# Performance work log

Hardware: AMD Instinct MI355X
Metric: run time of the kernel (lower is better)

The kernel has to match this reference:

```python
import jax, jax.numpy as jnp
import numpy as np

B, N, NC, T, C, H = 8, 16, 16, 64, 512, 8


def setup_inputs() -> dict:
    key = jax.random.key(0)
    ks = jax.random.split(key, 7)
    s = 1.0 / np.sqrt(C)  # ~kaiming-uniform scale for Linear weights
    x = jax.random.normal(ks[0], (B, N, T, C), dtype=jnp.float32)
    c = jax.random.normal(ks[1], (B, NC, T, C), dtype=jnp.float32)
    mask = jax.random.randint(ks[2], (B, N * T, (N + NC) * T), 0, 2).astype(bool)
    Wq = jax.random.normal(ks[3], (C, C), dtype=jnp.float32) * s  # [out, in], torch Linear layout
    Wk = jax.random.normal(ks[4], (C, C), dtype=jnp.float32) * s
    Wv = jax.random.normal(ks[5], (C, C), dtype=jnp.float32) * s
    Wp = jax.random.normal(ks[6], (C, C), dtype=jnp.float32) * s
    return {"x": x, "c": c, "mask": mask, "Wq": Wq, "Wk": Wk, "Wv": Wv, "Wp": Wp}


def reference(x, c, mask, Wq, Wk, Wv, Wp):
    Bx, Nx, Tx, Cx = x.shape
    Dh = Cx // H
    kv_in = jnp.concatenate([x, c], axis=1)           # hybrid: [B, N+NC, T, C]
    Nk = kv_in.shape[1]
    # torch Linear: y = x @ W.T  -> einsum '...c,dc->...d'
    q = jnp.einsum('bntc,dc->bntd', x, Wq).reshape(Bx, Nx * Tx, H, Dh).transpose(0, 2, 1, 3)
    k = jnp.einsum('bntc,dc->bntd', kv_in, Wk).reshape(Bx, Nk * Tx, H, Dh).transpose(0, 2, 1, 3)
    v = jnp.einsum('bntc,dc->bntd', kv_in, Wv).reshape(Bx, Nk * Tx, H, Dh).transpose(0, 2, 1, 3)
    att = jnp.einsum('bhqd,bhkd->bhqk', q, k) * (1.0 / np.sqrt(Dh))  # [B,H,NT,NkT]
    att = jnp.where(mask[:, None, :, :], -jnp.inf, att)
    att = jax.nn.softmax(att, axis=-1)
    y = jnp.einsum('bhqk,bhkd->bhqd', att, v)          # [B,H,NT,Dh]
    y = y.transpose(0, 2, 1, 3).reshape(Bx, Nx * Tx, Cx)
    y = jnp.einsum('btc,dc->btd', y, Wp)
    return y.reshape(Bx, Nx, Tx, Cx)
```

## Files before the change

kernel.cpp:

```cpp
#include <hip/hip_runtime.h>
#include <hip/hip_bf16.h>
#include <stdint.h>

typedef __bf16 v8bf __attribute__((ext_vector_type(8)));
typedef short v4s __attribute__((ext_vector_type(4)));
typedef float f32x4 __attribute__((ext_vector_type(4)));

__device__ __forceinline__ void gload_lds16(const void* g, void* l) {
    __builtin_amdgcn_global_load_lds(
        (const __attribute__((address_space(1))) void*)g,
        (__attribute__((address_space(3))) void*)l, 16, 0, 0);
}

__device__ __forceinline__ unsigned short f2bf(float f) {
    __hip_bfloat16 h = __float2bfloat16(f);
    return __builtin_bit_cast(unsigned short, h);
}

__device__ __forceinline__ float andf(float e, int m) {
    return __builtin_bit_cast(float, __builtin_bit_cast(unsigned int, e) & (unsigned int)m);
}

#define SBIT(w, off, ioff) (((int)((w) << (ioff))) >> 31)

#define WAITV4_BAR() asm volatile("s_waitcnt vmcnt(4)\n\ts_barrier" ::: "memory")
#define WAITV0_BAR() asm volatile("s_waitcnt vmcnt(0)\n\ts_barrier" ::: "memory")
#define RAW_BAR() asm volatile("s_barrier" ::: "memory")

__device__ __forceinline__ f32x4 mfma16x16x16bf(v4s a, v4s b, f32x4 c) {
#if __has_builtin(__builtin_amdgcn_mfma_f32_16x16x16bf16_1k)
    return __builtin_amdgcn_mfma_f32_16x16x16bf16_1k(a, b, c, 0, 0, 0);
#elif __has_builtin(__builtin_amdgcn_mfma_f32_16x16x16_bf16)
    return __builtin_amdgcn_mfma_f32_16x16x16_bf16(a, b, c, 0, 0, 0);
#else
    asm("s_nop 1\n\t"
        "v_mfma_f32_16x16x16_bf16 %0, %1, %2, %0\n\t"
        "s_nop 7\n\ts_nop 3"
        : "+v"(c) : "v"(a), "v"(b));
    return c;
#endif
}

__global__ __launch_bounds__(256) void cvt_xcw(const float* __restrict__ x,
                                               const float* __restrict__ c,
                                               const float* __restrict__ wq,
                                               const float* __restrict__ wk,
                                               const float* __restrict__ wv,
                                               const float* __restrict__ wp,
                                               __hip_bfloat16* __restrict__ xc,
                                               __hip_bfloat16* __restrict__ wout) {
    int bid = blockIdx.x;
    if (bid < 8192) {
        int i = bid * 256 + threadIdx.x;
        long e = (long)i * 4;
        int b = (int)(e >> 20);
        int rem = (int)(e & ((1 << 20) - 1));
        int r = rem >> 9;
        int col = rem & 511;
        const float* src = (r < 1024) ? (x + ((long)b << 19) + (long)r * 512 + col)
                                      : (c + ((long)b << 19) + (long)(r - 1024) * 512 + col);
        float4 v = *(const float4*)src;
        ushort4 o;
        o.x = f2bf(v.x); o.y = f2bf(v.y); o.z = f2bf(v.z); o.w = f2bf(v.w);
        ((ushort4*)xc)[i] = o;
    } else {
        int i = (bid - 8192) * 256 + threadIdx.x;
        int e = i * 4;
        int w = e >> 18;
        int off = e & ((1 << 18) - 1);
        const float* src = (w == 0 ? wq : w == 1 ? wk : w == 2 ? wv : wp) + off;
        float4 val = *(const float4*)src;
        ushort4 o;
        o.x = f2bf(val.x); o.y = f2bf(val.y); o.z = f2bf(val.z); o.w = f2bf(val.w);
        ((ushort4*)wout)[i] = o;
    }
}

__global__ __launch_bounds__(256) void cvt_mask(const int* __restrict__ mask,
                                                unsigned long long* __restrict__ mbt) {
    int t = threadIdx.x;
    long base = (long)blockIdx.x * 1024;
#pragma unroll
    for (int j = 0; j < 4; j++) {
        long i = base + j * 256 + t;
        int v = mask[i] != 0;
        unsigned long long bits = __ballot(v);
        if ((t & 63) == 0) {
            int b = (int)(i >> 21);
            int q = (int)((i >> 11) & 1023);
            int word = (int)((i >> 6) & 31);
            mbt[((long)b * 32 + word) * 1024 + q] = bits;
        }
    }
}

__global__ __launch_bounds__(256) void gemm_qkv(const __hip_bfloat16* __restrict__ A,
                                                const __hip_bfloat16* __restrict__ Bw,
                                                __hip_bfloat16* __restrict__ Qw,
                                                __hip_bfloat16* __restrict__ Kw,
                                                __hip_bfloat16* __restrict__ Vtw) {
    __shared__ union {
        struct { __hip_bfloat16 As[2][128 * 32]; __hip_bfloat16 Bs[2][128 * 32]; } s;
        __hip_bfloat16 T[64 * 136];
    } u;
    const int tid = threadIdx.x;
    const int wave = tid >> 6, lane = tid & 63;
    const int m0 = blockIdx.x * 128, n0 = blockIdx.y * 128;

    const int la = lane >> 2;
    const int kc = (lane & 3) * 8;
    const long ga0 = (long)(m0 + wave * 16 + la) * 512 + kc;
    const long ga1 = (long)(m0 + (wave + 4) * 16 + la) * 512 + kc;
    const long gb0 = (long)(n0 + wave * 16 + la) * 512 + kc;
    const long gb1 = (long)(n0 + (wave + 4) * 16 + la) * 512 + kc;

    f32x4 acc[4][4] = {};
    const int mw = (wave & 1) * 64, nw = (wave >> 1) * 64;
    const int lrow = lane & 15, lk = (lane >> 4) * 8;

    gload_lds16(A + ga0, &u.s.As[0][wave * 512]);
    gload_lds16(A + ga1, &u.s.As[0][(wave + 4) * 512]);
    gload_lds16(Bw + gb0, &u.s.Bs[0][wave * 512]);
    gload_lds16(Bw + gb1, &u.s.Bs[0][(wave + 4) * 512]);

    for (int it = 0; it < 16; ++it) {
        const int cur = it & 1;
        if (it < 15) {
            const int k0 = (it + 1) * 32;
            gload_lds16(A + ga0 + k0, &u.s.As[cur ^ 1][wave * 512]);
            gload_lds16(A + ga1 + k0, &u.s.As[cur ^ 1][(wave + 4) * 512]);
            gload_lds16(Bw + gb0 + k0, &u.s.Bs[cur ^ 1][wave * 512]);
            gload_lds16(Bw + gb1 + k0, &u.s.Bs[cur ^ 1][(wave + 4) * 512]);
            WAITV4_BAR();
        } else {
            WAITV0_BAR();
        }
        v8bf a[4], b[4];
#pragma unroll
        for (int i = 0; i < 4; i++) {
            a[i] = *(const v8bf*)&u.s.As[cur][(mw + i * 16 + lrow) * 32 + lk];
            b[i] = *(const v8bf*)&u.s.Bs[cur][(nw + i * 16 + lrow) * 32 + lk];
        }
        __builtin_amdgcn_s_setprio(1);
#pragma unroll
        for (int mi = 0; mi < 4; mi++)
#pragma unroll
            for (int ni = 0; ni < 4; ni++)
                acc[mi][ni] = __builtin_amdgcn_mfma_f32_16x16x32_bf16(a[mi], b[ni], acc[mi][ni], 0, 0, 0);
        __builtin_amdgcn_s_setprio(0);
        RAW_BAR();
    }

    const int lq = lane >> 4;
    if (blockIdx.y < 8) {
#pragma unroll
        for (int mi = 0; mi < 4; mi++)
#pragma unroll
            for (int ni = 0; ni < 4; ni++)
#pragma unroll
                for (int r = 0; r < 4; r++) {
                    int grow = m0 + mw + mi * 16 + lq * 4 + r;
                    int gcol = n0 + nw + ni * 16 + lrow;
                    int w = gcol >> 9, g9 = gcol & 511;
                    int h = g9 >> 6, dh = g9 & 63;
                    int b_ = grow >> 11, rr = grow & 2047;
                    float val = acc[mi][ni][r];
                    if (w == 0) {
                        if (rr < 1024)
                            Qw[((long)(b_ * 8 + h) * 1024 + rr) * 64 + dh] =
                                __float2bfloat16(val * 0.1803368801f);
                    } else {
                        Kw[((long)(b_ * 8 + h) * 2048 + rr) * 64 + dh] = __float2bfloat16(val);
                    }
                }
    } else {
        const int no = (blockIdx.y - 8) * 128;
        const int b_ = m0 >> 11, rrb = m0 & 2047;
#pragma unroll
        for (int pass = 0; pass < 2; ++pass) {
            __syncthreads();
            if ((wave >> 1) == pass) {
#pragma unroll
                for (int mi = 0; mi < 4; mi++)
#pragma unroll
                    for (int ni = 0; ni < 4; ni++) {
                        int n_l = ni * 16 + lrow;
                        int m_l = mw + mi * 16 + lq * 4;
                        ushort4 pk;
                        pk.x = f2bf(acc[mi][ni][0]); pk.y = f2bf(acc[mi][ni][1]);
                        pk.z = f2bf(acc[mi][ni][2]); pk.w = f2bf(acc[mi][ni][3]);
                        *(ushort4*)&u.T[n_l * 136 + m_l] = pk;
                    }
            }
            __syncthreads();
#pragma unroll
            for (int i = 0; i < 4; i++) {
                int sI = tid + i * 256;
                int n_l = sI >> 4, ch = sI & 15;
                int ng = no + pass * 64 + n_l;
                int h = ng >> 6, dh = ng & 63;
                uint4 v = *(const uint4*)&u.T[n_l * 136 + ch * 8];
                *(uint4*)&Vtw[((long)(b_ * 8 + h) * 64 + dh) * 2048 + rrb + ch * 8] = v;
            }
        }
    }
}

__global__ __launch_bounds__(256) void gemm_out(const __hip_bfloat16* __restrict__ A,
                                                const __hip_bfloat16* __restrict__ Bw,
                                                float* __restrict__ outp) {
    __shared__ __hip_bfloat16 As[2][128 * 32];
    __shared__ __hip_bfloat16 Bs[2][128 * 32];
    const int tid = threadIdx.x;
    const int wave = tid >> 6, lane = tid & 63;
    const int m0 = blockIdx.x * 128, n0 = blockIdx.y * 128;

    const int la = lane >> 2;
    const int kc = (lane & 3) * 8;
    const long ga0 = (long)(m0 + wave * 16 + la) * 512 + kc;
    const long ga1 = (long)(m0 + (wave + 4) * 16 + la) * 512 + kc;
    const long gb0 = (long)(n0 + wave * 16 + la) * 512 + kc;
    const long gb1 = (long)(n0 + (wave + 4) * 16 + la) * 512 + kc;

    f32x4 acc[4][4] = {};
    const int mw = (wave & 1) * 64, nw = (wave >> 1) * 64;
    const int lrow = lane & 15, lk = (lane >> 4) * 8;

    gload_lds16(A + ga0, &As[0][wave * 512]);
    gload_lds16(A + ga1, &As[0][(wave + 4) * 512]);
    gload_lds16(Bw + gb0, &Bs[0][wave * 512]);
    gload_lds16(Bw + gb1, &Bs[0][(wave + 4) * 512]);

    for (int it = 0; it < 16; ++it) {
        const int cur = it & 1;
        if (it < 15) {
            const int k0 = (it + 1) * 32;
            gload_lds16(A + ga0 + k0, &As[cur ^ 1][wave * 512]);
            gload_lds16(A + ga1 + k0, &As[cur ^ 1][(wave + 4) * 512]);
            gload_lds16(Bw + gb0 + k0, &Bs[cur ^ 1][wave * 512]);
            gload_lds16(Bw + gb1 + k0, &Bs[cur ^ 1][(wave + 4) * 512]);
            WAITV4_BAR();
        } else {
            WAITV0_BAR();
        }
        v8bf a[4], b[4];
#pragma unroll
        for (int i = 0; i < 4; i++) {
            a[i] = *(const v8bf*)&As[cur][(mw + i * 16 + lrow) * 32 + lk];
            b[i] = *(const v8bf*)&Bs[cur][(nw + i * 16 + lrow) * 32 + lk];
        }
        __builtin_amdgcn_s_setprio(1);
#pragma unroll
        for (int mi = 0; mi < 4; mi++)
#pragma unroll
            for (int ni = 0; ni < 4; ni++)
                acc[mi][ni] = __builtin_amdgcn_mfma_f32_16x16x32_bf16(a[mi], b[ni], acc[mi][ni], 0, 0, 0);
        __builtin_amdgcn_s_setprio(0);
        RAW_BAR();
    }

    const int lq = lane >> 4;
#pragma unroll
    for (int mi = 0; mi < 4; mi++)
#pragma unroll
        for (int ni = 0; ni < 4; ni++)
#pragma unroll
            for (int r = 0; r < 4; r++) {
                int grow = m0 + mw + mi * 16 + lq * 4 + r;
                int gcol = n0 + nw + ni * 16 + lrow;
                outp[(long)grow * 512 + gcol] = acc[mi][ni][r];
            }
}

__global__ __launch_bounds__(256) void flash(const __hip_bfloat16* __restrict__ Q,
                                             const __hip_bfloat16* __restrict__ K,
                                             const __hip_bfloat16* __restrict__ Vt,
                                             const unsigned long long* __restrict__ Mbt,
                                             __hip_bfloat16* __restrict__ Y) {
    constexpr int LDT = 72;
    __shared__ __hip_bfloat16 Ks[2][64 * LDT];
    __shared__ __hip_bfloat16 Vts[2][64 * LDT];

    const int L = blockIdx.x;
    const int b = L & 7, qt = (L >> 3) & 15, h = L >> 7;
    const int bh = b * 8 + h;
    const int tid = threadIdx.x, w = tid >> 6, lane = tid & 63;
    const int lcol = lane & 15, lq = lane >> 4;

    const __hip_bfloat16* Qp = Q + ((long)bh * 1024 + qt * 64 + w * 16 + lcol) * 64 + lq * 8;
    const __hip_bfloat16* Kg = K + (long)bh * 2048 * 64;
    const __hip_bfloat16* Vg = Vt + (long)bh * 64 * 2048;
    const unsigned long long* Mp = Mbt + (long)b * 32 * 1024 + qt * 64 + w * 16 + lcol;

    const int u0 = tid, u1 = tid + 256;
    const int r0 = u0 >> 3, p0 = u0 & 7;
    const int r1 = u1 >> 3, p1 = u1 & 7;

    int ioff[8];
#pragma unroll
    for (int jj = 0; jj < 8; jj++)
        ioff[jj] = 31 - ((jj >> 2) * 16 + lq * 4 + (jj & 3));

    v8bf bq0 = *(const v8bf*)(Qp);
    v8bf bq1 = *(const v8bf*)(Qp + 32);

    f32x4 O[4] = {};
    f32x4 Osum = {};
    const v4s bones = {(short)0x3F80, (short)0x3F80, (short)0x3F80, (short)0x3F80};

    unsigned long long mword = Mp[0];
    {
        const uint4* ksrc = (const uint4*)Kg;
        uint4 k0 = ksrc[u0], k1 = ksrc[u1];
        uint4 v0 = *(const uint4*)(Vg + (long)r0 * 2048 + p0 * 8);
        uint4 v1 = *(const uint4*)(Vg + (long)r1 * 2048 + p1 * 8);
        *(uint4*)&Ks[0][r0 * LDT + p0 * 8] = k0;
        *(uint4*)&Ks[0][r1 * LDT + p1 * 8] = k1;
        *(uint4*)&Vts[0][r0 * LDT + p0 * 8] = v0;
        *(uint4*)&Vts[0][r1 * LDT + p1 * 8] = v1;
    }
    __syncthreads();

    int cur = 0;
    for (int kt = 0; kt < 32; kt++) {
        const unsigned int kw_lo = ~(unsigned int)mword;
        const unsigned int kw_hi = ~(unsigned int)(mword >> 32);

        uint4 nk0, nk1, nv0, nv1;
        if (kt < 31) {
            const uint4* ksrc = (const uint4*)(Kg + ((kt + 1) << 12));
            nk0 = ksrc[u0];
            nk1 = ksrc[u1];
            nv0 = *(const uint4*)(Vg + (long)r0 * 2048 + (kt + 1) * 64 + p0 * 8);
            nv1 = *(const uint4*)(Vg + (long)r1 * 2048 + (kt + 1) * 64 + p1 * 8);
            mword = Mp[(long)(kt + 1) * 1024];
        }

        const __hip_bfloat16* Kb = Ks[cur];
        const __hip_bfloat16* Vb = Vts[cur];
#pragma unroll
        for (int nt = 0; nt < 4; nt++) {
            v8bf ak0 = *(const v8bf*)&Kb[(nt * 16 + lcol) * LDT + lq * 8];
            v8bf ak1 = *(const v8bf*)&Kb[(nt * 16 + lcol) * LDT + 32 + lq * 8];
            f32x4 st = {};
            __builtin_amdgcn_s_setprio(1);
            st = __builtin_amdgcn_mfma_f32_16x16x32_bf16(ak0, bq0, st, 0, 0, 0);
            st = __builtin_amdgcn_mfma_f32_16x16x32_bf16(ak1, bq1, st, 0, 0, 0);
            __builtin_amdgcn_s_setprio(0);
            const unsigned int kw = (nt < 2) ? kw_lo : kw_hi;
            const int base = (nt & 1) * 4;
            float e0 = andf(__builtin_amdgcn_exp2f(st[0]), SBIT(kw, , ioff[base + 0]));
            float e1 = andf(__builtin_amdgcn_exp2f(st[1]), SBIT(kw, , ioff[base + 1]));
            float e2 = andf(__builtin_amdgcn_exp2f(st[2]), SBIT(kw, , ioff[base + 2]));
            float e3 = andf(__builtin_amdgcn_exp2f(st[3]), SBIT(kw, , ioff[base + 3]));
            __hip_bfloat162 lo = __float22bfloat162_rn(make_float2(e0, e1));
            __hip_bfloat162 hi = __float22bfloat162_rn(make_float2(e2, e3));
            uint2 pku;
            __builtin_memcpy(&pku.x, &lo, 4);
            __builtin_memcpy(&pku.y, &hi, 4);
            v4s pa = __builtin_bit_cast(v4s, pku);
            __builtin_amdgcn_s_setprio(1);
            Osum = mfma16x16x16bf(pa, bones, Osum);
#pragma unroll
            for (int nd = 0; nd < 4; nd++) {
                v4s bv = *(const v4s*)&Vb[(nd * 16 + lcol) * LDT + nt * 16 + lq * 4];
                O[nd] = mfma16x16x16bf(pa, bv, O[nd]);
            }
            __builtin_amdgcn_s_setprio(0);
        }

        if (kt < 31) {
            __hip_bfloat16* Kw_ = Ks[cur ^ 1];
            __hip_bfloat16* Vw_ = Vts[cur ^ 1];
            *(uint4*)&Kw_[r0 * LDT + p0 * 8] = nk0;
            *(uint4*)&Kw_[r1 * LDT + p1 * 8] = nk1;
            *(uint4*)&Vw_[r0 * LDT + p0 * 8] = nv0;
            *(uint4*)&Vw_[r1 * LDT + p1 * 8] = nv1;
        }
        __syncthreads();
        cur ^= 1;
    }

    float inv[4];
#pragma unroll
    for (int r = 0; r < 4; r++) inv[r] = 1.f / Osum[r];

    __hip_bfloat16* Yp = Y + ((long)b * 1024 + qt * 64 + w * 16) * 512 + h * 64 + lcol;
#pragma unroll
    for (int nd = 0; nd < 4; nd++)
#pragma unroll
        for (int r = 0; r < 4; r++)
            Yp[(long)(lq * 4 + r) * 512 + nd * 16] = __float2bfloat16(O[nd][r] * inv[r]);
}

extern "C" void kernel_launch(void* const* d_in, const int* in_sizes, int n_in,
                              void* d_out, int out_size, void* d_ws, size_t ws_size,
                              hipStream_t stream) {
    const float* x = (const float*)d_in[0];
    const float* c = (const float*)d_in[1];
    const int* mask = (const int*)d_in[2];
    const float* Wq = (const float*)d_in[3];
    const float* Wk = (const float*)d_in[4];
    const float* Wv = (const float*)d_in[5];
    const float* Wp = (const float*)d_in[6];

    char* ws = (char*)d_ws;
    __hip_bfloat16* xc  = (__hip_bfloat16*)(ws);
    __hip_bfloat16* Wbf = (__hip_bfloat16*)(ws + 16777216);
    __hip_bfloat16* Qw  = (__hip_bfloat16*)(ws + 18874368);
    __hip_bfloat16* Kw  = (__hip_bfloat16*)(ws + 27262976);
    __hip_bfloat16* Vtw = (__hip_bfloat16*)(ws + 44040192);
    __hip_bfloat16* Yb  = (__hip_bfloat16*)(ws + 60817408);
    unsigned long long* Mbp = (unsigned long long*)(ws);

    cvt_xcw<<<9216, 256, 0, stream>>>(x, c, Wq, Wk, Wv, Wp, xc, Wbf);
    gemm_qkv<<<dim3(128, 12), 256, 0, stream>>>(xc, Wbf, Qw, Kw, Vtw);
    cvt_mask<<<16384, 256, 0, stream>>>(mask, Mbp);
    flash<<<1024, 256, 0, stream>>>(Qw, Kw, Vtw, Mbp, Yb);
    gemm_out<<<dim3(64, 4), 256, 0, stream>>>(Yb, Wbf + 3 * 262144, (float*)d_out);
}
```

Measured before the change: 262.1 us.

## Load K tiles directly into swizzled LDS and compute softmax row sums with shuffles

The projection kernel now writes K with an XOR chunk swizzle per row, so the flash kernel can copy K tiles straight from global to LDS with global_load_lds. This removes the register staging and LDS stores for K and avoids bank conflicts without padding. The softmax denominator is now accumulated in scalar registers and reduced with cross-lane shuffles, replacing an extra MFMA per tile. Vt loading stays register-staged, and the direct LDS loads rely on the existing barrier for completion.

```diff
diff --git a/kernel.cpp b/kernel.cpp
--- a/kernel.cpp
+++ b/kernel.cpp
@@ -21,7 +21,7 @@
     return __builtin_bit_cast(float, __builtin_bit_cast(unsigned int, e) & (unsigned int)m);
 }
 
-#define SBIT(w, off, ioff) (((int)((w) << (ioff))) >> 31)
+#define SBIT(w, ioff) (((int)((w) << (ioff))) >> 31)
 
 #define WAITV4_BAR() asm volatile("s_waitcnt vmcnt(4)\n\ts_barrier" ::: "memory")
 #define WAITV0_BAR() asm volatile("s_waitcnt vmcnt(0)\n\ts_barrier" ::: "memory")
@@ -170,7 +170,8 @@
                             Qw[((long)(b_ * 8 + h) * 1024 + rr) * 64 + dh] =
                                 __float2bfloat16(val * 0.1803368801f);
                     } else {
-                        Kw[((long)(b_ * 8 + h) * 2048 + rr) * 64 + dh] = __float2bfloat16(val);
+                        Kw[((long)(b_ * 8 + h) * 2048 + rr) * 64 + (dh ^ ((rr & 7) << 3))] =
+                            __float2bfloat16(val);
                     }
                 }
     } else {
@@ -278,7 +279,7 @@
                                              const unsigned long long* __restrict__ Mbt,
                                              __hip_bfloat16* __restrict__ Y) {
     constexpr int LDT = 72;
-    __shared__ __hip_bfloat16 Ks[2][64 * LDT];
+    __shared__ __hip_bfloat16 KsL[2][64 * 64];
     __shared__ __hip_bfloat16 Vts[2][64 * LDT];
 
     const int L = blockIdx.x;
@@ -292,30 +293,35 @@
     const __hip_bfloat16* Vg = Vt + (long)bh * 64 * 2048;
     const unsigned long long* Mp = Mbt + (long)b * 32 * 1024 + qt * 64 + w * 16 + lcol;
 
-    const int u0 = tid, u1 = tid + 256;
-    const int r0 = u0 >> 3, p0 = u0 & 7;
+    const int u1 = tid + 256;
+    const int r0 = tid >> 3, p0 = tid & 7;
     const int r1 = u1 >> 3, p1 = u1 & 7;
+    const __hip_bfloat16* Vp0 = Vg + (long)r0 * 2048 + p0 * 8;
+    const __hip_bfloat16* Vp1 = Vg + (long)r1 * 2048 + p1 * 8;
+
+    const __hip_bfloat16* Kc0 = Kg + (w * 64 + lane) * 8;
+    const __hip_bfloat16* Kc1 = Kc0 + 2048;
 
     int ioff[8];
 #pragma unroll
     for (int jj = 0; jj < 8; jj++)
         ioff[jj] = 31 - ((jj >> 2) * 16 + lq * 4 + (jj & 3));
 
+    const int ksw0 = (lq ^ (lcol & 7)) * 8;
+    const int ksw1 = ((lq + 4) ^ (lcol & 7)) * 8;
+
     v8bf bq0 = *(const v8bf*)(Qp);
     v8bf bq1 = *(const v8bf*)(Qp + 32);
 
     f32x4 O[4] = {};
-    f32x4 Osum = {};
-    const v4s bones = {(short)0x3F80, (short)0x3F80, (short)0x3F80, (short)0x3F80};
+    float lsum = 0.f;
 
     unsigned long long mword = Mp[0];
     {
-        const uint4* ksrc = (const uint4*)Kg;
-        uint4 k0 = ksrc[u0], k1 = ksrc[u1];
-        uint4 v0 = *(const uint4*)(Vg + (long)r0 * 2048 + p0 * 8);
-        uint4 v1 = *(const uint4*)(Vg + (long)r1 * 2048 + p1 * 8);
-        *(uint4*)&Ks[0][r0 * LDT + p0 * 8] = k0;
-        *(uint4*)&Ks[0][r1 * LDT + p1 * 8] = k1;
+        gload_lds16(Kc0, &KsL[0][w * 512]);
+        gload_lds16(Kc1, &KsL[0][2048 + w * 512]);
+        uint4 v0 = *(const uint4*)(Vp0);
+        uint4 v1 = *(const uint4*)(Vp1);
         *(uint4*)&Vts[0][r0 * LDT + p0 * 8] = v0;
         *(uint4*)&Vts[0][r1 * LDT + p1 * 8] = v1;
     }
@@ -326,22 +332,22 @@
         const unsigned int kw_lo = ~(unsigned int)mword;
         const unsigned int kw_hi = ~(unsigned int)(mword >> 32);
 
-        uint4 nk0, nk1, nv0, nv1;
+        uint4 nv0, nv1;
         if (kt < 31) {
-            const uint4* ksrc = (const uint4*)(Kg + ((kt + 1) << 12));
-            nk0 = ksrc[u0];
-            nk1 = ksrc[u1];
-            nv0 = *(const uint4*)(Vg + (long)r0 * 2048 + (kt + 1) * 64 + p0 * 8);
-            nv1 = *(const uint4*)(Vg + (long)r1 * 2048 + (kt + 1) * 64 + p1 * 8);
+            gload_lds16(Kc0 + (kt + 1) * 4096, &KsL[cur ^ 1][w * 512]);
+            gload_lds16(Kc1 + (kt + 1) * 4096, &KsL[cur ^ 1][2048 + w * 512]);
+            nv0 = *(const uint4*)(Vp0 + (kt + 1) * 64);
+            nv1 = *(const uint4*)(Vp1 + (kt + 1) * 64);
             mword = Mp[(long)(kt + 1) * 1024];
         }
 
-        const __hip_bfloat16* Kb = Ks[cur];
+        const __hip_bfloat16* Kb = KsL[cur];
         const __hip_bfloat16* Vb = Vts[cur];
 #pragma unroll
         for (int nt = 0; nt < 4; nt++) {
-            v8bf ak0 = *(const v8bf*)&Kb[(nt * 16 + lcol) * LDT + lq * 8];
-            v8bf ak1 = *(const v8bf*)&Kb[(nt * 16 + lcol) * LDT + 32 + lq * 8];
+            const int rowb = (nt * 16 + lcol) * 64;
+            v8bf ak0 = *(const v8bf*)&Kb[rowb + ksw0];
+            v8bf ak1 = *(const v8bf*)&Kb[rowb + ksw1];
             f32x4 st = {};
             __builtin_amdgcn_s_setprio(1);
             st = __builtin_amdgcn_mfma_f32_16x16x32_bf16(ak0, bq0, st, 0, 0, 0);
@@ -349,10 +355,11 @@
             __builtin_amdgcn_s_setprio(0);
             const unsigned int kw = (nt < 2) ? kw_lo : kw_hi;
             const int base = (nt & 1) * 4;
-            float e0 = andf(__builtin_amdgcn_exp2f(st[0]), SBIT(kw, , ioff[base + 0]));
-            float e1 = andf(__builtin_amdgcn_exp2f(st[1]), SBIT(kw, , ioff[base + 1]));
-            float e2 = andf(__builtin_amdgcn_exp2f(st[2]), SBIT(kw, , ioff[base + 2]));
-            float e3 = andf(__builtin_amdgcn_exp2f(st[3]), SBIT(kw, , ioff[base + 3]));
+            float e0 = andf(__builtin_amdgcn_exp2f(st[0]), SBIT(kw, ioff[base + 0]));
+            float e1 = andf(__builtin_amdgcn_exp2f(st[1]), SBIT(kw, ioff[base + 1]));
+            float e2 = andf(__builtin_amdgcn_exp2f(st[2]), SBIT(kw, ioff[base + 2]));
+            float e3 = andf(__builtin_amdgcn_exp2f(st[3]), SBIT(kw, ioff[base + 3]));
+            lsum += (e0 + e1) + (e2 + e3);
             __hip_bfloat162 lo = __float22bfloat162_rn(make_float2(e0, e1));
             __hip_bfloat162 hi = __float22bfloat162_rn(make_float2(e2, e3));
             uint2 pku;
@@ -360,7 +367,6 @@
             __builtin_memcpy(&pku.y, &hi, 4);
             v4s pa = __builtin_bit_cast(v4s, pku);
             __builtin_amdgcn_s_setprio(1);
-            Osum = mfma16x16x16bf(pa, bones, Osum);
 #pragma unroll
             for (int nd = 0; nd < 4; nd++) {
                 v4s bv = *(const v4s*)&Vb[(nd * 16 + lcol) * LDT + nt * 16 + lq * 4];
@@ -370,10 +376,7 @@
         }
 
         if (kt < 31) {
-            __hip_bfloat16* Kw_ = Ks[cur ^ 1];
             __hip_bfloat16* Vw_ = Vts[cur ^ 1];
-            *(uint4*)&Kw_[r0 * LDT + p0 * 8] = nk0;
-            *(uint4*)&Kw_[r1 * LDT + p1 * 8] = nk1;
             *(uint4*)&Vw_[r0 * LDT + p0 * 8] = nv0;
             *(uint4*)&Vw_[r1 * LDT + p1 * 8] = nv1;
         }
@@ -381,9 +384,12 @@
         cur ^= 1;
     }
 
+    float s = lsum;
+    s += __shfl_xor(s, 16);
+    s += __shfl_xor(s, 32);
     float inv[4];
 #pragma unroll
-    for (int r = 0; r < 4; r++) inv[r] = 1.f / Osum[r];
+    for (int r = 0; r < 4; r++) inv[r] = 1.f / __shfl(s, lq * 4 + r);
 
     __hip_bfloat16* Yp = Y + ((long)b * 1024 + qt * 64 + w * 16) * 512 + h * 64 + lcol;
 #pragma unroll
```

Result: slower. 271.5 us (+3.6%).

## Stage Q/K epilogue through LDS, skip dead Q tiles, sum softmax denominators in VALU

Applied to the files above, without the earlier changes.

The Q/K epilogue of the QKV GEMM is staged through a padded LDS tile so global stores are 16-byte vectors instead of scattered 2-byte writes. Q-column blocks whose rows fall in the context half now exit early instead of computing and discarding. In attention, the row-sum MFMA against a ones vector is replaced by an fp32 VALU accumulation plus cross-lane shuffles. The mask bits are inverted at conversion time so a single v_bfe_i32 produces the keep-mask directly. The costs are an extra LDS round trip and barriers in the epilogue, and per-element adds and shuffles in the attention loop.

```diff
diff --git a/kernel.cpp b/kernel.cpp
--- a/kernel.cpp
+++ b/kernel.cpp
@@ -5,6 +5,7 @@
 typedef __bf16 v8bf __attribute__((ext_vector_type(8)));
 typedef short v4s __attribute__((ext_vector_type(4)));
 typedef float f32x4 __attribute__((ext_vector_type(4)));
+typedef float f32x2 __attribute__((ext_vector_type(2)));
 
 __device__ __forceinline__ void gload_lds16(const void* g, void* l) {
     __builtin_amdgcn_global_load_lds(
@@ -21,7 +22,11 @@
     return __builtin_bit_cast(float, __builtin_bit_cast(unsigned int, e) & (unsigned int)m);
 }
 
-#define SBIT(w, off, ioff) (((int)((w) << (ioff))) >> 31)
+__device__ __forceinline__ int sbit(unsigned int w, int off) {
+    int m;
+    asm("v_bfe_i32 %0, %1, %2, 1" : "=v"(m) : "v"(w), "v"(off));
+    return m;
+}
 
 #define WAITV4_BAR() asm volatile("s_waitcnt vmcnt(4)\n\ts_barrier" ::: "memory")
 #define WAITV0_BAR() asm volatile("s_waitcnt vmcnt(0)\n\ts_barrier" ::: "memory")
@@ -83,7 +88,7 @@
 #pragma unroll
     for (int j = 0; j < 4; j++) {
         long i = base + j * 256 + t;
-        int v = mask[i] != 0;
+        int v = mask[i] == 0;
         unsigned long long bits = __ballot(v);
         if ((t & 63) == 0) {
             int b = (int)(i >> 21);
@@ -101,11 +106,15 @@
                                                 __hip_bfloat16* __restrict__ Vtw) {
     __shared__ union {
         struct { __hip_bfloat16 As[2][128 * 32]; __hip_bfloat16 Bs[2][128 * 32]; } s;
-        __hip_bfloat16 T[64 * 136];
+        __hip_bfloat16 T[64 * 138];
     } u;
     const int tid = threadIdx.x;
     const int wave = tid >> 6, lane = tid & 63;
     const int m0 = blockIdx.x * 128, n0 = blockIdx.y * 128;
+
+    const bool isQ = (blockIdx.y < 4);
+    const int rr_base = m0 & 2047;
+    if (isQ && rr_base >= 1024) return;
 
     const int la = lane >> 2;
     const int kc = (lane & 3) * 8;
@@ -152,30 +161,43 @@
     }
 
     const int lq = lane >> 4;
+    const int b_ = m0 >> 11;
     if (blockIdx.y < 8) {
-#pragma unroll
-        for (int mi = 0; mi < 4; mi++)
-#pragma unroll
-            for (int ni = 0; ni < 4; ni++)
-#pragma unroll
-                for (int r = 0; r < 4; r++) {
-                    int grow = m0 + mw + mi * 16 + lq * 4 + r;
-                    int gcol = n0 + nw + ni * 16 + lrow;
-                    int w = gcol >> 9, g9 = gcol & 511;
-                    int h = g9 >> 6, dh = g9 & 63;
-                    int b_ = grow >> 11, rr = grow & 2047;
-                    float val = acc[mi][ni][r];
-                    if (w == 0) {
-                        if (rr < 1024)
-                            Qw[((long)(b_ * 8 + h) * 1024 + rr) * 64 + dh] =
-                                __float2bfloat16(val * 0.1803368801f);
-                    } else {
-                        Kw[((long)(b_ * 8 + h) * 2048 + rr) * 64 + dh] = __float2bfloat16(val);
+        const float qs = isQ ? 0.1803368801f : 1.f;
+#pragma unroll
+        for (int pass = 0; pass < 2; ++pass) {
+            if (pass) __syncthreads();
+            if ((wave & 1) == pass) {
+#pragma unroll
+                for (int mi = 0; mi < 4; mi++)
+#pragma unroll
+                    for (int ni = 0; ni < 4; ni++) {
+                        const int nl = nw + ni * 16 + lrow;
+#pragma unroll
+                        for (int r = 0; r < 4; r++)
+                            u.T[(mi * 16 + lq * 4 + r) * 138 + nl] =
+                                __float2bfloat16(acc[mi][ni][r] * qs);
                     }
-                }
+            }
+            __syncthreads();
+#pragma unroll
+            for (int i = 0; i < 4; i++) {
+                int sI = tid + i * 256;
+                int row = sI >> 4, ch = sI & 15;
+                int grow = m0 + pass * 64 + row;
+                int rr = grow & 2047;
+                int gcol = n0 + ch * 8;
+                int h = (gcol & 511) >> 6, dh = gcol & 63;
+                uint4 v = *(const uint4*)&u.T[row * 138 + ch * 8];
+                if (isQ)
+                    *(uint4*)&Qw[((long)(b_ * 8 + h) * 1024 + rr) * 64 + dh] = v;
+                else
+                    *(uint4*)&Kw[((long)(b_ * 8 + h) * 2048 + rr) * 64 + dh] = v;
+            }
+        }
     } else {
         const int no = (blockIdx.y - 8) * 128;
-        const int b_ = m0 >> 11, rrb = m0 & 2047;
+        const int rrb = m0 & 2047;
 #pragma unroll
         for (int pass = 0; pass < 2; ++pass) {
             __syncthreads();
@@ -296,17 +318,16 @@
     const int r0 = u0 >> 3, p0 = u0 & 7;
     const int r1 = u1 >> 3, p1 = u1 & 7;
 
-    int ioff[8];
+    int boff[8];
 #pragma unroll
     for (int jj = 0; jj < 8; jj++)
-        ioff[jj] = 31 - ((jj >> 2) * 16 + lq * 4 + (jj & 3));
+        boff[jj] = (jj >> 2) * 16 + lq * 4 + (jj & 3);
 
     v8bf bq0 = *(const v8bf*)(Qp);
     v8bf bq1 = *(const v8bf*)(Qp + 32);
 
     f32x4 O[4] = {};
-    f32x4 Osum = {};
-    const v4s bones = {(short)0x3F80, (short)0x3F80, (short)0x3F80, (short)0x3F80};
+    f32x2 ls = {0.f, 0.f};
 
     unsigned long long mword = Mp[0];
     {
@@ -323,8 +344,8 @@
 
     int cur = 0;
     for (int kt = 0; kt < 32; kt++) {
-        const unsigned int kw_lo = ~(unsigned int)mword;
-        const unsigned int kw_hi = ~(unsigned int)(mword >> 32);
+        const unsigned int kw_lo = (unsigned int)mword;
+        const unsigned int kw_hi = (unsigned int)(mword >> 32);
 
         uint4 nk0, nk1, nv0, nv1;
         if (kt < 31) {
@@ -349,10 +370,11 @@
             __builtin_amdgcn_s_setprio(0);
             const unsigned int kw = (nt < 2) ? kw_lo : kw_hi;
             const int base = (nt & 1) * 4;
-            float e0 = andf(__builtin_amdgcn_exp2f(st[0]), SBIT(kw, , ioff[base + 0]));
-            float e1 = andf(__builtin_amdgcn_exp2f(st[1]), SBIT(kw, , ioff[base + 1]));
-            float e2 = andf(__builtin_amdgcn_exp2f(st[2]), SBIT(kw, , ioff[base + 2]));
-            float e3 = andf(__builtin_amdgcn_exp2f(st[3]), SBIT(kw, , ioff[base + 3]));
+            float e0 = andf(__builtin_amdgcn_exp2f(st[0]), sbit(kw, boff[base + 0]));
+            float e1 = andf(__builtin_amdgcn_exp2f(st[1]), sbit(kw, boff[base + 1]));
+            float e2 = andf(__builtin_amdgcn_exp2f(st[2]), sbit(kw, boff[base + 2]));
+            float e3 = andf(__builtin_amdgcn_exp2f(st[3]), sbit(kw, boff[base + 3]));
+            ls += (f32x2){e0, e1} + (f32x2){e2, e3};
             __hip_bfloat162 lo = __float22bfloat162_rn(make_float2(e0, e1));
             __hip_bfloat162 hi = __float22bfloat162_rn(make_float2(e2, e3));
             uint2 pku;
@@ -360,7 +382,6 @@
             __builtin_memcpy(&pku.y, &hi, 4);
             v4s pa = __builtin_bit_cast(v4s, pku);
             __builtin_amdgcn_s_setprio(1);
-            Osum = mfma16x16x16bf(pa, bones, Osum);
 #pragma unroll
             for (int nd = 0; nd < 4; nd++) {
                 v4s bv = *(const v4s*)&Vb[(nd * 16 + lcol) * LDT + nt * 16 + lq * 4];
@@ -381,9 +402,12 @@
         cur ^= 1;
     }
 
+    float s = ls[0] + ls[1];
+    s += __shfl_xor(s, 16);
+    s += __shfl_xor(s, 32);
     float inv[4];
 #pragma unroll
-    for (int r = 0; r < 4; r++) inv[r] = 1.f / Osum[r];
+    for (int r = 0; r < 4; r++) inv[r] = 1.f / __shfl(s, lq * 4 + r);
 
     __hip_bfloat16* Yp = Y + ((long)b * 1024 + qt * 64 + w * 16) * 512 + h * 64 + lcol;
 #pragma unroll
```

Measured after the change: 260.2 us. No clear change (-0.7%).
